# Kernel tuning notes

Hardware: AMD Instinct MI355X
Metric: run time of the kernel (lower is better)

Reference implementation:

```python
import jax, jax.numpy as jnp
import numpy as np

N_NODES = 100000
N_EDGES = 800000
VOCAB = 256      # node_dict_size
NODE_DIM = 256
HIDDEN = 256
N_MASK = 10000


def setup_inputs() -> dict:
    key = jax.random.key(0)
    ks = jax.random.split(key, 8)
    return {
        "x": jax.random.randint(ks[0], (N_NODES, 1), 0, VOCAB, dtype=jnp.int64 if jax.config.jax_enable_x64 else jnp.int32),
        "edge_index": jax.random.randint(ks[1], (2, N_EDGES), 0, N_NODES, dtype=jnp.int32),
        "mask_x_position": jax.random.randint(ks[2], (N_MASK,), 0, N_NODES, dtype=jnp.int32),
        "emb": jax.random.normal(ks[3], (VOCAB, NODE_DIM), dtype=jnp.float32) * (NODE_DIM ** -0.5),
        "W1": jax.random.normal(ks[4], (NODE_DIM, HIDDEN), dtype=jnp.float32) * (NODE_DIM ** -0.5),
        "b1": jnp.zeros((HIDDEN,), dtype=jnp.float32),
        "W2": jax.random.normal(ks[5], (HIDDEN, VOCAB), dtype=jnp.float32) * (HIDDEN ** -0.5),
        "b2": jnp.zeros((VOCAB,), dtype=jnp.float32),
    }


def _gcn_conv(h, W, b, src, dst, norm, n_nodes):
    # PyG GCNConv: out = scatter_add(norm * (h @ W)[src], dst) + b
    hw = h @ W                                      # [N, out]
    msgs = hw[src] * norm[:, None]                  # [E+N, out]
    out = jax.ops.segment_sum(msgs, dst, num_segments=n_nodes)
    return out + b


def _gcn_norm(edge_index, n_nodes):
    # add self-loops, compute sym-normalized edge weights (PyG gcn_norm)
    loops = jnp.arange(n_nodes, dtype=edge_index.dtype)
    src = jnp.concatenate([edge_index[0], loops])
    dst = jnp.concatenate([edge_index[1], loops])
    deg = jax.ops.segment_sum(jnp.ones_like(dst, dtype=jnp.float32), dst,
                              num_segments=n_nodes)  # in-degree incl. self-loop
    dinv = jnp.where(deg > 0, jax.lax.rsqrt(deg), 0.0)
    norm = dinv[src] * dinv[dst]                    # [E+N]
    return src, dst, norm


def reference(x, edge_index, mask_x_position, emb, W1, b1, W2, b2):
    n_nodes = x.shape[0]
    src, dst, norm = _gcn_norm(edge_index, n_nodes)
    h = emb[x[:, 0]]                                # Embedding + squeeze(1) -> [N, node_dim]
    # dropout p=0 / eval mode -> identity
    h = _gcn_conv(h, W1, b1, src, dst, norm, n_nodes)
    h = jax.nn.relu(h)
    h = _gcn_conv(h, W2, b2, src, dst, norm, n_nodes)  # [N, vocab]
    return jax.nn.log_softmax(h[mask_x_position], axis=1)
```

## Files before the change

kernel.cpp:

```cpp
#include <hip/hip_runtime.h>
#include <stdint.h>

#define NN 100000
#define NE 800000
#define ND 256
#define NM 10000
#define NMP 10048
#define NPB 128
#define NBK 782
#define BCAP 1280
#define TILE 1024
#define EBK ((NE + TILE - 1) / TILE)

typedef __attribute__((ext_vector_type(8))) short bf16x8;
typedef __attribute__((ext_vector_type(4))) float f32x4;

__device__ __forceinline__ float bf2f(unsigned short u) {
    return __uint_as_float(((unsigned)u) << 16);
}
__device__ __forceinline__ unsigned short f2bf(float f) {
    unsigned u = __float_as_uint(f);
    u += 0x7fffu + ((u >> 16) & 1u);
    return (unsigned short)(u >> 16);
}


__global__ void k_maskmap(const int* __restrict__ mpos, int* __restrict__ minfo,
                          unsigned char* __restrict__ mb, unsigned char* __restrict__ fb,
                          int* __restrict__ gcur, int* __restrict__ nctr) {
    int j = blockIdx.x * 256 + threadIdx.x;
    if (j < NM) {
        int p = mpos[j];
        minfo[p] = (j + 1) << 1;
        mb[p] = 1;
        fb[p] = 1;
    }
    if (j < NBK) gcur[j] = j * BCAP;
    if (j == 0) *nctr = 0;
}

__global__ __launch_bounds__(256) void k_bin(
    const int* __restrict__ src, const int* __restrict__ dst,
    const unsigned char* __restrict__ mb, unsigned char* __restrict__ fb,
    int* __restrict__ gcur, int* __restrict__ ebuf,
    const float* __restrict__ emb, const float* __restrict__ W1,
    const float* __restrict__ W2,
    unsigned short* __restrict__ M1, unsigned short* __restrict__ W2t) {
    __shared__ int lcnt[NBK];
    __shared__ int sd[TILE], ss[TILE];
    __shared__ float er[ND];
    int b = blockIdx.x, t = threadIdx.x;
    if (b >= EBK) {
        int bb = b - EBK;
        if (bb < ND) {
            er[t] = emb[bb * ND + t];
            __syncthreads();
            float acc = 0.f;
            for (int k = 0; k < ND; k++) acc += er[k] * W1[k * ND + t];
            M1[bb * ND + t] = f2bf(acc);
        } else {
            int n = bb - ND;
            W2t[n * ND + t] = f2bf(W2[t * ND + n]);
        }
        return;
    }
    for (int i = t; i < NBK; i += 256) lcnt[i] = 0;
    __syncthreads();
    int e0 = b * TILE;
#pragma unroll
    for (int k = 0; k < TILE / 256; k++) {
        int idx = t + k * 256;
        int e = e0 + idx;
        if (e < NE) {
            int d = dst[e], s = src[e];
            sd[idx] = d; ss[idx] = s;
            atomicAdd(&lcnt[d >> 7], 1);
            if (mb[d] == 1) fb[s] = 1;
        }
    }
    __syncthreads();
    for (int i = t; i < NBK; i += 256) {
        int c = lcnt[i];
        lcnt[i] = c ? atomicAdd(&gcur[i], c) : 0;
    }
    __syncthreads();
    int nv = min(NE - e0, TILE);
#pragma unroll
    for (int k = 0; k < TILE / 256; k++) {
        int idx = t + k * 256;
        if (idx < nv) {
            int d = sd[idx], s = ss[idx];
            int bk = d >> 7, j = d & 127;
            int pos = atomicAdd(&lcnt[bk], 1);
            if (pos < (bk + 1) * BCAP) ebuf[pos] = s | (j << 17);
        }
    }
}

__global__ void k_bhist(const int* __restrict__ gcur, const int* __restrict__ ebuf,
                        const int* __restrict__ x, const unsigned char* __restrict__ mb,
                        const unsigned char* __restrict__ fb,
                        int* __restrict__ carr, int4* __restrict__ xd4,
                        int* __restrict__ nlist, int* __restrict__ nctr,
                        int* __restrict__ part) {
    __shared__ int bins[NPB];
    __shared__ int rs[4];
    int b = blockIdx.x, t = threadIdx.x;
    int lane = t & 63, wv = t >> 6;
    if (t < NPB) bins[t] = 0;
    __syncthreads();
    int n = min(gcur[b] - b * BCAP, BCAP);
    int base = b * BCAP;
    for (int i = t; i < n; i += 256)
        atomicAdd(&bins[ebuf[base + i] >> 17], 1);
    __syncthreads();
    int node = b * NPB + t;
    int w = 0;
    if (t < NPB && node < NN) {
        int c = bins[t];
        carr[node] = c;
        float dv = rsqrtf((float)c + 1.0f);
        int cc = 0;
        if (fb[node] == 1) {
            cc = atomicAdd(nctr, 1);
            nlist[cc] = node;
        }
        xd4[node] = make_int4(x[node], __float_as_int(dv), cc, 0);
        w = c + ((mb[node] == 1) ? c : 0);
    }
#pragma unroll
    for (int o = 32; o >= 1; o >>= 1) w += __shfl_xor(w, o, 64);
    if (lane == 0) rs[wv] = w;
    __syncthreads();
    if (t == 0) part[b] = rs[0] + rs[1] + rs[2] + rs[3];
}

__global__ __launch_bounds__(256) void k_place(
    const int* __restrict__ gcur, const int* __restrict__ ebuf,
    const int* __restrict__ minfo, const unsigned char* __restrict__ fb,
    const int* __restrict__ carr, const int* __restrict__ part,
    const int4* __restrict__ xd4, int* __restrict__ off, int2* __restrict__ pairs,
    int4* __restrict__ nrec) {
    __shared__ int sinfo[NPB], lc1[NPB], lc2[NPB];
    __shared__ int bred[4], wtot[2];
    int b = blockIdx.x, t = threadIdx.x;
    int lane = t & 63, wv = t >> 6;
    int pv = 0;
    for (int i = t; i < b; i += 256) pv += part[i];
#pragma unroll
    for (int o = 32; o >= 1; o >>= 1) pv += __shfl_xor(pv, o, 64);
    if (lane == 0) bred[wv] = pv;
    __syncthreads();
    int pbase = bred[0] + bred[1] + bred[2] + bred[3];
    int node = b * NPB + t;
    int c = 0, m = 0, f = 0;
    if (t < NPB && node < NN) {
        c = carr[node];
        int mv = minfo[node];
        if (mv > 0) m = mv;
        f = (fb[node] == 1) ? 1 : 0;
    }
    int wgt = (t < NPB) ? (c + (m ? c : 0)) : 0;
    int xx = wgt;
    for (int o = 1; o < 64; o <<= 1) { int y = __shfl_up(xx, o, 64); if (lane >= o) xx += y; }
    if (lane == 63 && wv < 2) wtot[wv] = xx;
    __syncthreads();
    if (t < NPB) {
        int excl = xx - wgt + ((wv == 1) ? wtot[0] : 0);
        int myoff = pbase + excl;
        if (node < NN) {
            off[node] = myoff;
            if (f) {
                int4 xv = xd4[node];
                nrec[xv.z] = make_int4(xv.x, xv.y, myoff, c);
            }
        }
        sinfo[t] = m | f;
        lc1[t] = myoff;
        lc2[t] = myoff + c;
    }
    __syncthreads();
    int n = min(gcur[b] - b * BCAP, BCAP);
    int base = b * BCAP;
    for (int i = t; i < n; i += 256) {
        int w = ebuf[base + i];
        int j = w >> 17, s = w & 0x1FFFF;
        int ii = sinfo[j];
        if (ii == 0) continue;
        int4 xv = xd4[s];
        if (ii & 1) {
            int p = atomicAdd(&lc1[j], 1);
            pairs[p] = make_int2(xv.x, xv.y);
        }
        if (ii > 1) {
            int p = atomicAdd(&lc2[j], 1);
            pairs[p] = make_int2(xv.z, xv.y);
        }
    }
}

__global__ __launch_bounds__(1024) void k_expand(
    const int* __restrict__ nctr, const int4* __restrict__ nrec,
    const int2* __restrict__ pairs,
    const unsigned short* __restrict__ M1,
    const float* __restrict__ b1,
    unsigned short* __restrict__ h1c) {
    __shared__ unsigned short sm1[ND * ND];
    int t = threadIdx.x;
    {
        const uint4* g = (const uint4*)M1;
        uint4* s = (uint4*)sm1;
        for (int i = t; i < (ND * ND) / 8; i += 1024) s[i] = g[i];
    }
    __syncthreads();
    int lane = t & 63;
    float4 b1v = ((const float4*)b1)[lane];
    int nw = nctr[0];
    for (int idx = (blockIdx.x * 1024 + t) >> 6; idx < nw; idx += 4096) {
        int4 rec = nrec[idx];
        int v0 = rec.x;
        float w0 = __int_as_float(rec.y);
        ushort4 mm = *(const ushort4*)(sm1 + v0 * ND + lane * 4);
        float a0 = w0 * bf2f(mm.x), a1 = w0 * bf2f(mm.y);
        float a2 = w0 * bf2f(mm.z), a3 = w0 * bf2f(mm.w);
        int e = rec.z, end = e + rec.w;
        for (; e + 4 <= end; e += 4) {
            int2 pA = pairs[e + 0];
            int2 pB = pairs[e + 1];
            int2 pC = pairs[e + 2];
            int2 pD = pairs[e + 3];
            ushort4 mA = *(const ushort4*)(sm1 + pA.x * ND + lane * 4);
            ushort4 mB = *(const ushort4*)(sm1 + pB.x * ND + lane * 4);
            ushort4 mC = *(const ushort4*)(sm1 + pC.x * ND + lane * 4);
            ushort4 mD = *(const ushort4*)(sm1 + pD.x * ND + lane * 4);
            float wA = __int_as_float(pA.y), wB = __int_as_float(pB.y);
            float wC = __int_as_float(pC.y), wD = __int_as_float(pD.y);
            a0 += wA * bf2f(mA.x) + wB * bf2f(mB.x) + wC * bf2f(mC.x) + wD * bf2f(mD.x);
            a1 += wA * bf2f(mA.y) + wB * bf2f(mB.y) + wC * bf2f(mC.y) + wD * bf2f(mD.y);
            a2 += wA * bf2f(mA.z) + wB * bf2f(mB.z) + wC * bf2f(mC.z) + wD * bf2f(mD.z);
            a3 += wA * bf2f(mA.w) + wB * bf2f(mB.w) + wC * bf2f(mC.w) + wD * bf2f(mD.w);
        }
        for (; e < end; e++) {
            int2 p = pairs[e];
            float w = __int_as_float(p.y);
            ushort4 m2 = *(const ushort4*)(sm1 + p.x * ND + lane * 4);
            a0 += w * bf2f(m2.x);
            a1 += w * bf2f(m2.y);
            a2 += w * bf2f(m2.z);
            a3 += w * bf2f(m2.w);
        }
        ushort4 o;
        o.x = f2bf(fmaxf(fmaf(w0, a0, b1v.x), 0.f));
        o.y = f2bf(fmaxf(fmaf(w0, a1, b1v.y), 0.f));
        o.z = f2bf(fmaxf(fmaf(w0, a2, b1v.z), 0.f));
        o.w = f2bf(fmaxf(fmaf(w0, a3, b1v.w), 0.f));
        ((ushort4*)(h1c + (size_t)idx * ND))[lane] = o;
    }
}

__global__ void k_agg2(const int* __restrict__ mpos, const int* __restrict__ minfo,
                       const int4* __restrict__ xd4,
                       const int2* __restrict__ pairs, const int* __restrict__ off,
                       const int* __restrict__ carr,
                       const unsigned short* __restrict__ h1c,
                       unsigned short* __restrict__ agg2b) {
    int lane = threadIdx.x & 63;
    int wave = (blockIdx.x * 256 + threadIdx.x) >> 6;
    if (wave >= NM) return;
    int r = wave;
    int p = mpos[r];
    if ((minfo[p] >> 1) != r + 1) return;
    int4 xp = xd4[p];
    int cp = xp.z;
    float dv = __int_as_float(xp.y);
    ushort4 h0 = *(const ushort4*)(h1c + (size_t)cp * ND + lane * 4);
    float a0 = dv * bf2f(h0.x), a1 = dv * bf2f(h0.y);
    float a2 = dv * bf2f(h0.z), a3 = dv * bf2f(h0.w);
    int c2 = carr[p];
    int e = off[p] + c2, end = e + c2;
    for (; e + 4 <= end; e += 4) {
        int2 pA = pairs[e + 0];
        int2 pB = pairs[e + 1];
        int2 pC = pairs[e + 2];
        int2 pD = pairs[e + 3];
        ushort4 hA = *(const ushort4*)(h1c + (size_t)pA.x * ND + lane * 4);
        ushort4 hB = *(const ushort4*)(h1c + (size_t)pB.x * ND + lane * 4);
        ushort4 hC = *(const ushort4*)(h1c + (size_t)pC.x * ND + lane * 4);
        ushort4 hD = *(const ushort4*)(h1c + (size_t)pD.x * ND + lane * 4);
        float wA = __int_as_float(pA.y), wB = __int_as_float(pB.y);
        float wC = __int_as_float(pC.y), wD = __int_as_float(pD.y);
        a0 += wA * bf2f(hA.x) + wB * bf2f(hB.x) + wC * bf2f(hC.x) + wD * bf2f(hD.x);
        a1 += wA * bf2f(hA.y) + wB * bf2f(hB.y) + wC * bf2f(hC.y) + wD * bf2f(hD.y);
        a2 += wA * bf2f(hA.z) + wB * bf2f(hB.z) + wC * bf2f(hC.z) + wD * bf2f(hD.z);
        a3 += wA * bf2f(hA.w) + wB * bf2f(hB.w) + wC * bf2f(hC.w) + wD * bf2f(hD.w);
    }
    for (; e < end; e++) {
        int2 pp = pairs[e];
        float w = __int_as_float(pp.y);
        ushort4 hv = *(const ushort4*)(h1c + (size_t)pp.x * ND + lane * 4);
        a0 += w * bf2f(hv.x);
        a1 += w * bf2f(hv.y);
        a2 += w * bf2f(hv.z);
        a3 += w * bf2f(hv.w);
    }
    ushort4 o;
    o.x = f2bf(dv * a0);
    o.y = f2bf(dv * a1);
    o.z = f2bf(dv * a2);
    o.w = f2bf(dv * a3);
    ((ushort4*)(agg2b + (size_t)r * ND))[lane] = o;
}

__global__ __launch_bounds__(256) void k_out2(
    const int* __restrict__ mpos, const int* __restrict__ minfo,
    const unsigned short* __restrict__ agg2b, const unsigned short* __restrict__ W2t,
    const float* __restrict__ b2, float* __restrict__ out) {
    int lane = threadIdx.x & 63;
    int wv = threadIdx.x >> 6;
    int row0 = blockIdx.x * 64 + wv * 16;
    int qm = lane & 15, qk = lane >> 4;
    int row = row0 + qm;
    bf16x8 afr[8];
    if (row < NM) {
        int p = mpos[row];
        int rr = (minfo[p] >> 1) - 1;
        const unsigned short* arow = agg2b + (size_t)rr * ND + qk * 8;
#pragma unroll
        for (int kt = 0; kt < 8; kt++) afr[kt] = *(const bf16x8*)(arow + kt * 32);
    } else {
#pragma unroll
        for (int kt = 0; kt < 8; kt++) afr[kt] = (bf16x8){0, 0, 0, 0, 0, 0, 0, 0};
    }
    f32x4 acc[16];
#pragma unroll
    for (int t = 0; t < 16; t++) acc[t] = (f32x4){0.f, 0.f, 0.f, 0.f};
#pragma unroll
    for (int t = 0; t < 16; t++) {
        const unsigned short* brow = W2t + (size_t)(t * 16 + qm) * ND + qk * 8;
#pragma unroll
        for (int kt = 0; kt < 8; kt++) {
            bf16x8 bfr = *(const bf16x8*)(brow + kt * 32);
            acc[t] = __builtin_amdgcn_mfma_f32_16x16x32_bf16(afr[kt], bfr, acc[t], 0, 0, 0);
        }
    }
    float mx[4] = {-1e30f, -1e30f, -1e30f, -1e30f};
#pragma unroll
    for (int t = 0; t < 16; t++) {
        float cb = b2[qm + 16 * t];
#pragma unroll
        for (int r = 0; r < 4; r++) {
            float v = acc[t][r] + cb;
            acc[t][r] = v;
            mx[r] = fmaxf(mx[r], v);
        }
    }
#pragma unroll
    for (int r = 0; r < 4; r++)
        for (int o = 1; o < 16; o <<= 1) mx[r] = fmaxf(mx[r], __shfl_xor(mx[r], o, 64));
    float sm[4] = {0.f, 0.f, 0.f, 0.f};
#pragma unroll
    for (int t = 0; t < 16; t++)
#pragma unroll
        for (int r = 0; r < 4; r++) sm[r] += __expf(acc[t][r] - mx[r]);
#pragma unroll
    for (int r = 0; r < 4; r++)
        for (int o = 1; o < 16; o <<= 1) sm[r] += __shfl_xor(sm[r], o, 64);
#pragma unroll
    for (int r = 0; r < 4; r++) {
        int orow_i = row0 + qk * 4 + r;
        if (orow_i >= NM) continue;
        float lse = mx[r] + __logf(sm[r]);
        float* orow = out + (size_t)orow_i * ND + qm;
#pragma unroll
        for (int t = 0; t < 16; t++) orow[16 * t] = acc[t][r] - lse;
    }
}

extern "C" void kernel_launch(void* const* d_in, const int* in_sizes, int n_in,
                              void* d_out, int out_size, void* d_ws, size_t ws_size,
                              hipStream_t stream) {
    const int* x    = (const int*)d_in[0];
    const int* ei   = (const int*)d_in[1];
    const int* src  = ei;
    const int* dst  = ei + NE;
    const int* mpos = (const int*)d_in[2];
    const float* emb = (const float*)d_in[3];
    const float* W1  = (const float*)d_in[4];
    const float* b1  = (const float*)d_in[5];
    const float* W2  = (const float*)d_in[6];
    const float* b2  = (const float*)d_in[7];
    float* out = (float*)d_out;

    char* w = (char*)d_ws;
    size_t o = 0;
#define ALLOC(nbytes) ({ void* _p = (void*)(w + o); o = (o + (size_t)(nbytes) + 63) & ~(size_t)63; _p; })
    int*   carr  = (int*)ALLOC((size_t)(NN + 64) * 4);
    int*   off   = (int*)ALLOC((size_t)(NN + 64) * 4);
    int*   minfo = (int*)ALLOC((size_t)NN * 4);
    unsigned char* mb = (unsigned char*)ALLOC(NN + 64);
    unsigned char* fb = (unsigned char*)ALLOC(NN + 64);
    int4*  xd4   = (int4*)ALLOC((size_t)NN * 16);
    int*   nlist = (int*)ALLOC((size_t)NN * 4);
    int*   nctr  = (int*)ALLOC(64);
    int*   part  = (int*)ALLOC(1024 * 4);
    int*   gcur  = (int*)ALLOC((size_t)(NBK + 64) * 4);
    int*   ebuf  = (int*)ALLOC((size_t)NBK * BCAP * 4);
    unsigned short* M1    = (unsigned short*)ALLOC((size_t)ND * ND * 2);
    unsigned short* W2t   = (unsigned short*)ALLOC((size_t)ND * ND * 2);
    unsigned short* agg2b = (unsigned short*)ALLOC((size_t)NM * ND * 2);
    int2*  pairs = (int2*)ALLOC((size_t)NE * 2 * 8);
    int4*  nrec  = (int4*)ALLOC((size_t)NN * 16);
    unsigned short* h1c  = (unsigned short*)ALLOC((size_t)NN * ND * 2);
#undef ALLOC

    k_maskmap<<<(NM + 255) / 256, 256, 0, stream>>>(mpos, minfo, mb, fb, gcur, nctr);
    k_bin<<<EBK + 2 * ND, 256, 0, stream>>>(src, dst, mb, fb, gcur, ebuf,
                                            emb, W1, W2, M1, W2t);
    k_bhist<<<NBK, 256, 0, stream>>>(gcur, ebuf, x, mb, fb, carr, xd4, nlist, nctr, part);
    k_place<<<NBK, 256, 0, stream>>>(gcur, ebuf, minfo, fb, carr, part, xd4, off, pairs, nrec);
    k_expand<<<256, 1024, 0, stream>>>(nctr, nrec, pairs, M1, b1, h1c);
    k_agg2<<<(NM + 3) / 4, 256, 0, stream>>>(mpos, minfo, xd4, pairs, off, carr, h1c, agg2b);
    k_out2<<<NMP / 64, 256, 0, stream>>>(mpos, minfo, agg2b, W2t, b2, out);
}
```

Measured before the change: 201.6 us.

## Enlarge destination bins to 256 nodes, pad bin cursors, drop unused node list

Node bins now cover 256 destinations each instead of 128, so there are half as many bins and each block in the histogram and placement kernels uses all 256 threads. Edge tiles in the binning kernel grow to 4096 edges, which cuts the number of global cursor atomics per bin. Each global cursor is padded to its own 64-byte slot to avoid false sharing between atomics. The unused nlist write is removed. In exchange, fewer blocks run the bhist and place kernels, which lowers parallelism, and each binning block needs more shared memory.

```diff
diff --git a/kernel.cpp b/kernel.cpp
--- a/kernel.cpp
+++ b/kernel.cpp
@@ -6,10 +6,10 @@
 #define ND 256
 #define NM 10000
 #define NMP 10048
-#define NPB 128
-#define NBK 782
-#define BCAP 1280
-#define TILE 1024
+#define NPB 256
+#define NBK 391
+#define BCAP 2560
+#define TILE 4096
 #define EBK ((NE + TILE - 1) / TILE)
 
 typedef __attribute__((ext_vector_type(8))) short bf16x8;
@@ -35,7 +35,7 @@
         mb[p] = 1;
         fb[p] = 1;
     }
-    if (j < NBK) gcur[j] = j * BCAP;
+    if (j < NBK) gcur[j << 4] = j * BCAP;
     if (j == 0) *nctr = 0;
 }
 
@@ -74,14 +74,14 @@
         if (e < NE) {
             int d = dst[e], s = src[e];
             sd[idx] = d; ss[idx] = s;
-            atomicAdd(&lcnt[d >> 7], 1);
+            atomicAdd(&lcnt[d >> 8], 1);
             if (mb[d] == 1) fb[s] = 1;
         }
     }
     __syncthreads();
     for (int i = t; i < NBK; i += 256) {
         int c = lcnt[i];
-        lcnt[i] = c ? atomicAdd(&gcur[i], c) : 0;
+        lcnt[i] = c ? atomicAdd(&gcur[i << 4], c) : 0;
     }
     __syncthreads();
     int nv = min(NE - e0, TILE);
@@ -90,7 +90,7 @@
         int idx = t + k * 256;
         if (idx < nv) {
             int d = sd[idx], s = ss[idx];
-            int bk = d >> 7, j = d & 127;
+            int bk = d >> 8, j = d & 255;
             int pos = atomicAdd(&lcnt[bk], 1);
             if (pos < (bk + 1) * BCAP) ebuf[pos] = s | (j << 17);
         }
@@ -101,30 +101,26 @@
                         const int* __restrict__ x, const unsigned char* __restrict__ mb,
                         const unsigned char* __restrict__ fb,
                         int* __restrict__ carr, int4* __restrict__ xd4,
-                        int* __restrict__ nlist, int* __restrict__ nctr,
-                        int* __restrict__ part) {
+                        int* __restrict__ nctr, int* __restrict__ part) {
     __shared__ int bins[NPB];
     __shared__ int rs[4];
     int b = blockIdx.x, t = threadIdx.x;
     int lane = t & 63, wv = t >> 6;
-    if (t < NPB) bins[t] = 0;
-    __syncthreads();
-    int n = min(gcur[b] - b * BCAP, BCAP);
+    bins[t] = 0;
+    __syncthreads();
+    int n = min(gcur[b << 4] - b * BCAP, BCAP);
     int base = b * BCAP;
     for (int i = t; i < n; i += 256)
         atomicAdd(&bins[ebuf[base + i] >> 17], 1);
     __syncthreads();
     int node = b * NPB + t;
     int w = 0;
-    if (t < NPB && node < NN) {
+    if (node < NN) {
         int c = bins[t];
         carr[node] = c;
         float dv = rsqrtf((float)c + 1.0f);
         int cc = 0;
-        if (fb[node] == 1) {
-            cc = atomicAdd(nctr, 1);
-            nlist[cc] = node;
-        }
+        if (fb[node] == 1) cc = atomicAdd(nctr, 1);
         xd4[node] = make_int4(x[node], __float_as_int(dv), cc, 0);
         w = c + ((mb[node] == 1) ? c : 0);
     }
@@ -142,7 +138,7 @@
     const int4* __restrict__ xd4, int* __restrict__ off, int2* __restrict__ pairs,
     int4* __restrict__ nrec) {
     __shared__ int sinfo[NPB], lc1[NPB], lc2[NPB];
-    __shared__ int bred[4], wtot[2];
+    __shared__ int bred[4], wtot[4];
     int b = blockIdx.x, t = threadIdx.x;
     int lane = t & 63, wv = t >> 6;
     int pv = 0;
@@ -154,33 +150,34 @@
     int pbase = bred[0] + bred[1] + bred[2] + bred[3];
     int node = b * NPB + t;
     int c = 0, m = 0, f = 0;
-    if (t < NPB && node < NN) {
+    if (node < NN) {
         c = carr[node];
         int mv = minfo[node];
         if (mv > 0) m = mv;
         f = (fb[node] == 1) ? 1 : 0;
     }
-    int wgt = (t < NPB) ? (c + (m ? c : 0)) : 0;
+    int wgt = c + (m ? c : 0);
     int xx = wgt;
     for (int o = 1; o < 64; o <<= 1) { int y = __shfl_up(xx, o, 64); if (lane >= o) xx += y; }
-    if (lane == 63 && wv < 2) wtot[wv] = xx;
-    __syncthreads();
-    if (t < NPB) {
-        int excl = xx - wgt + ((wv == 1) ? wtot[0] : 0);
-        int myoff = pbase + excl;
-        if (node < NN) {
-            off[node] = myoff;
-            if (f) {
-                int4 xv = xd4[node];
-                nrec[xv.z] = make_int4(xv.x, xv.y, myoff, c);
-            }
-        }
-        sinfo[t] = m | f;
-        lc1[t] = myoff;
-        lc2[t] = myoff + c;
-    }
-    __syncthreads();
-    int n = min(gcur[b] - b * BCAP, BCAP);
+    if (lane == 63) wtot[wv] = xx;
+    __syncthreads();
+    int wadd = 0;
+#pragma unroll
+    for (int k = 0; k < 4; k++) if (k < wv) wadd += wtot[k];
+    int excl = xx - wgt + wadd;
+    int myoff = pbase + excl;
+    if (node < NN) {
+        off[node] = myoff;
+        if (f) {
+            int4 xv = xd4[node];
+            nrec[xv.z] = make_int4(xv.x, xv.y, myoff, c);
+        }
+    }
+    sinfo[t] = m | f;
+    lc1[t] = myoff;
+    lc2[t] = myoff + c;
+    __syncthreads();
+    int n = min(gcur[b << 4] - b * BCAP, BCAP);
     int base = b * BCAP;
     for (int i = t; i < n; i += 256) {
         int w = ebuf[base + i];
@@ -400,10 +397,9 @@
     unsigned char* mb = (unsigned char*)ALLOC(NN + 64);
     unsigned char* fb = (unsigned char*)ALLOC(NN + 64);
     int4*  xd4   = (int4*)ALLOC((size_t)NN * 16);
-    int*   nlist = (int*)ALLOC((size_t)NN * 4);
     int*   nctr  = (int*)ALLOC(64);
-    int*   part  = (int*)ALLOC(1024 * 4);
-    int*   gcur  = (int*)ALLOC((size_t)(NBK + 64) * 4);
+    int*   part  = (int*)ALLOC(512 * 4);
+    int*   gcur  = (int*)ALLOC((size_t)(NBK * 16 + 64) * 4);
     int*   ebuf  = (int*)ALLOC((size_t)NBK * BCAP * 4);
     unsigned short* M1    = (unsigned short*)ALLOC((size_t)ND * ND * 2);
     unsigned short* W2t   = (unsigned short*)ALLOC((size_t)ND * ND * 2);
@@ -416,7 +412,7 @@
     k_maskmap<<<(NM + 255) / 256, 256, 0, stream>>>(mpos, minfo, mb, fb, gcur, nctr);
     k_bin<<<EBK + 2 * ND, 256, 0, stream>>>(src, dst, mb, fb, gcur, ebuf,
                                             emb, W1, W2, M1, W2t);
-    k_bhist<<<NBK, 256, 0, stream>>>(gcur, ebuf, x, mb, fb, carr, xd4, nlist, nctr, part);
+    k_bhist<<<NBK, 256, 0, stream>>>(gcur, ebuf, x, mb, fb, carr, xd4, nctr, part);
     k_place<<<NBK, 256, 0, stream>>>(gcur, ebuf, minfo, fb, carr, part, xd4, off, pairs, nrec);
     k_expand<<<256, 1024, 0, stream>>>(nctr, nrec, pairs, M1, b1, h1c);
     k_agg2<<<(NM + 3) / 4, 256, 0, stream>>>(mpos, minfo, xd4, pairs, off, carr, h1c, agg2b);
```

Result: faster. 190.6 us (-5.5%).
